# Optimization experiments

Measured on AMD Instinct MI355X. Metric: run time of the kernel, lower is better.

Reference implementation:

```python
import jax, jax.numpy as jnp
import numpy as np

R = 5.0      # cutoff radius (init arg)
N = 4096     # total atoms
B = 8        # number of periodic systems in the batch


def setup_inputs() -> dict:
    key = jax.random.key(0)
    k1, k2, k3 = jax.random.split(key, 3)
    # positions in a ~20 Angstrom box (matches cell scale)
    pos = jax.random.uniform(k1, (N, 3), dtype=jnp.float32) * 20.0
    # sorted per-atom graph ids, as produced by a batched molecular loader
    batch = jnp.sort(jax.random.randint(k2, (N,), 0, B))
    # near-cubic 20A cells with small triclinic perturbation (well-conditioned)
    cell = jnp.eye(3, dtype=jnp.float32) * 20.0 + 0.5 * jax.random.normal(k3, (B, 3, 3), dtype=jnp.float32)
    return {"pos": pos, "cell": cell, "batch": batch}


def reference(pos, cell, batch):
    # Dense, fixed-shape equivalent of RadiusGraph.forward with PBC cell wrap.
    # Original returns dynamically filtered (edge_index, disp); here we return
    # the full [N,N,3] displacement grid (masked to 0 off-graph) plus the
    # boolean edge mask -- same math, jit-compatible static shapes.
    n = pos.shape[0]
    disp = pos[:, None, :] - pos[None, :, :]            # [N,N,3], row i minus col j
    # PBC minimum-image wrap: per edge, cell is taken from the ROW node's graph
    cell_n = cell[batch]                                # [N,3,3]
    inv_cellT = jnp.linalg.inv(jnp.swapaxes(cell_n, 1, 2))   # [N,3,3] = (cell^T)^{-1}
    # scaled = solve(cell^T, disp) vectorized over all pairs
    scaled = jnp.einsum('iab,ijb->ija', inv_cellT, disp)     # [N,N,3]
    disp = disp - jnp.einsum('iab,ijb->ija', cell_n, jnp.round(scaled))
    # edge validity: same graph, no self-loop, within cutoff (after wrap)
    same_graph = batch[:, None] == batch[None, :]
    not_self = ~jnp.eye(n, dtype=bool)
    mask = same_graph & not_self & (jnp.linalg.norm(disp, axis=-1) < R)
    disp = jnp.where(mask[..., None], disp, jnp.zeros((), disp.dtype))
    return disp, mask
```

## Files before the change

kernel.cpp:

```cpp
#include <hip/hip_runtime.h>
#include <math.h>

#define NATOMS 4096
#define R_CUT 5.0f
#define BLOCK 256
#define GRID 2048
#define TPR (NATOMS / BLOCK)
#define NTILE (NATOMS * TPR)

typedef float f3 __attribute__((ext_vector_type(3), aligned(4)));

__global__ __launch_bounds__(BLOCK) void radius_graph_kernel(
    const float* __restrict__ pos,
    const float* __restrict__ cell,
    const int*   __restrict__ batch,
    float* __restrict__ disp_out,
    float* __restrict__ mask_out)
{
    const int tid = (int)threadIdx.x;

    for (int T = (int)blockIdx.x; T < NTILE; T += GRID) {
        const int i  = T >> 4;
        const int jb = T & (TPR - 1);
        const int j  = jb * BLOCK + tid;

        const int bi = batch[i];
        const float pix = pos[i * 3 + 0];
        const float piy = pos[i * 3 + 1];
        const float piz = pos[i * 3 + 2];

        const float* C = cell + (size_t)bi * 9;
        const float C00 = C[0], C01 = C[1], C02 = C[2];
        const float C10 = C[3], C11 = C[4], C12 = C[5];
        const float C20 = C[6], C21 = C[7], C22 = C[8];
        const float cof00 =  (C11 * C22 - C12 * C21);
        const float cof01 = -(C10 * C22 - C12 * C20);
        const float cof02 =  (C10 * C21 - C11 * C20);
        const float cof10 = -(C01 * C22 - C02 * C21);
        const float cof11 =  (C00 * C22 - C02 * C20);
        const float cof12 = -(C00 * C21 - C01 * C20);
        const float cof20 =  (C01 * C12 - C02 * C11);
        const float cof21 = -(C00 * C12 - C02 * C10);
        const float cof22 =  (C00 * C11 - C01 * C10);
        const float det = C00 * cof00 + C01 * cof01 + C02 * cof02;
        const float id  = 1.0f / det;
        const float A00 = cof00 * id, A01 = cof01 * id, A02 = cof02 * id;
        const float A10 = cof10 * id, A11 = cof11 * id, A12 = cof12 * id;
        const float A20 = cof20 * id, A21 = cof21 * id, A22 = cof22 * id;

        const float pjx = pos[j * 3 + 0];
        const float pjy = pos[j * 3 + 1];
        const float pjz = pos[j * 3 + 2];
        const int   bjv = batch[j];

        const float d0 = __fsub_rn(pix, pjx);
        const float d1 = __fsub_rn(piy, pjy);
        const float d2 = __fsub_rn(piz, pjz);

        const float s0 = __fadd_rn(__fadd_rn(__fmul_rn(A00, d0), __fmul_rn(A01, d1)), __fmul_rn(A02, d2));
        const float s1 = __fadd_rn(__fadd_rn(__fmul_rn(A10, d0), __fmul_rn(A11, d1)), __fmul_rn(A12, d2));
        const float s2 = __fadd_rn(__fadd_rn(__fmul_rn(A20, d0), __fmul_rn(A21, d1)), __fmul_rn(A22, d2));

        const float r0 = rintf(s0);
        const float r1 = rintf(s1);
        const float r2 = rintf(s2);

        const float w0 = __fsub_rn(d0, __fadd_rn(__fadd_rn(__fmul_rn(C00, r0), __fmul_rn(C01, r1)), __fmul_rn(C02, r2)));
        const float w1 = __fsub_rn(d1, __fadd_rn(__fadd_rn(__fmul_rn(C10, r0), __fmul_rn(C11, r1)), __fmul_rn(C12, r2)));
        const float w2 = __fsub_rn(d2, __fadd_rn(__fadd_rn(__fmul_rn(C20, r0), __fmul_rn(C21, r1)), __fmul_rn(C22, r2)));

        const float n2 = __fadd_rn(__fadd_rn(__fmul_rn(w0, w0), __fmul_rn(w1, w1)), __fmul_rn(w2, w2));
        const bool m = (bi == bjv) && (i != j) && (sqrtf(n2) < R_CUT);

        f3 v;
        v.x = m ? w0 : 0.0f;
        v.y = m ? w1 : 0.0f;
        v.z = m ? w2 : 0.0f;
        *(f3*)(disp_out + (size_t)T * (BLOCK * 3) + (size_t)tid * 3) = v;
        mask_out[(size_t)T * BLOCK + tid] = m ? 1.0f : 0.0f;
    }
}

extern "C" void kernel_launch(void* const* d_in, const int* in_sizes, int n_in,
                              void* d_out, int out_size, void* d_ws, size_t ws_size,
                              hipStream_t stream) {
    const float* pos   = (const float*)d_in[0];
    const float* cell  = (const float*)d_in[1];
    const int*   batch = (const int*)d_in[2];

    float* disp_out = (float*)d_out;
    float* mask_out = (float*)d_out + (size_t)NATOMS * NATOMS * 3;

    radius_graph_kernel<<<GRID, BLOCK, 0, stream>>>(pos, cell, batch, disp_out, mask_out);
}
```

Baseline: 262.7 us.

## Zero output with vectorized memset kernel, then scatter only valid edges

Splits the work into two kernels. The first bulk-zeroes the whole output with 16-byte stores. The second computes each row, skips pairs from different graphs, and writes displacement and mask only for edges within the cutoff. This replaces the dense 3-float unaligned stores with wide zero stores plus sparse scattered writes. The cost is an extra kernel launch and uncoalesced scattered stores.

```diff
diff --git a/kernel.cpp b/kernel.cpp
--- a/kernel.cpp
+++ b/kernel.cpp
@@ -4,54 +4,66 @@
 #define NATOMS 4096
 #define R_CUT 5.0f
 #define BLOCK 256
-#define GRID 2048
-#define TPR (NATOMS / BLOCK)
-#define NTILE (NATOMS * TPR)
 
+typedef float f4 __attribute__((ext_vector_type(4)));
 typedef float f3 __attribute__((ext_vector_type(3), aligned(4)));
 
-__global__ __launch_bounds__(BLOCK) void radius_graph_kernel(
+__global__ __launch_bounds__(BLOCK) void zero_kernel(f4* __restrict__ out, int n16)
+{
+    const int stride = (int)gridDim.x * BLOCK;
+    int idx = (int)blockIdx.x * BLOCK + (int)threadIdx.x;
+    const f4 z = {0.0f, 0.0f, 0.0f, 0.0f};
+    for (; idx < n16; idx += stride)
+        out[idx] = z;
+}
+
+__global__ __launch_bounds__(BLOCK) void sparse_kernel(
     const float* __restrict__ pos,
     const float* __restrict__ cell,
     const int*   __restrict__ batch,
     float* __restrict__ disp_out,
     float* __restrict__ mask_out)
 {
+    const int i   = (int)blockIdx.x;
     const int tid = (int)threadIdx.x;
 
-    for (int T = (int)blockIdx.x; T < NTILE; T += GRID) {
-        const int i  = T >> 4;
-        const int jb = T & (TPR - 1);
-        const int j  = jb * BLOCK + tid;
+    const int bi = batch[i];
+    const float pix = pos[i * 3 + 0];
+    const float piy = pos[i * 3 + 1];
+    const float piz = pos[i * 3 + 2];
 
-        const int bi = batch[i];
-        const float pix = pos[i * 3 + 0];
-        const float piy = pos[i * 3 + 1];
-        const float piz = pos[i * 3 + 2];
+    const float* C = cell + (size_t)bi * 9;
+    const float C00 = C[0], C01 = C[1], C02 = C[2];
+    const float C10 = C[3], C11 = C[4], C12 = C[5];
+    const float C20 = C[6], C21 = C[7], C22 = C[8];
+    const float cof00 =  (C11 * C22 - C12 * C21);
+    const float cof01 = -(C10 * C22 - C12 * C20);
+    const float cof02 =  (C10 * C21 - C11 * C20);
+    const float cof10 = -(C01 * C22 - C02 * C21);
+    const float cof11 =  (C00 * C22 - C02 * C20);
+    const float cof12 = -(C00 * C21 - C01 * C20);
+    const float cof20 =  (C01 * C12 - C02 * C11);
+    const float cof21 = -(C00 * C12 - C02 * C10);
+    const float cof22 =  (C00 * C11 - C01 * C10);
+    const float det = C00 * cof00 + C01 * cof01 + C02 * cof02;
+    const float id  = 1.0f / det;
+    const float A00 = cof00 * id, A01 = cof01 * id, A02 = cof02 * id;
+    const float A10 = cof10 * id, A11 = cof11 * id, A12 = cof12 * id;
+    const float A20 = cof20 * id, A21 = cof21 * id, A22 = cof22 * id;
 
-        const float* C = cell + (size_t)bi * 9;
-        const float C00 = C[0], C01 = C[1], C02 = C[2];
-        const float C10 = C[3], C11 = C[4], C12 = C[5];
-        const float C20 = C[6], C21 = C[7], C22 = C[8];
-        const float cof00 =  (C11 * C22 - C12 * C21);
-        const float cof01 = -(C10 * C22 - C12 * C20);
-        const float cof02 =  (C10 * C21 - C11 * C20);
-        const float cof10 = -(C01 * C22 - C02 * C21);
-        const float cof11 =  (C00 * C22 - C02 * C20);
-        const float cof12 = -(C00 * C21 - C01 * C20);
-        const float cof20 =  (C01 * C12 - C02 * C11);
-        const float cof21 = -(C00 * C12 - C02 * C10);
-        const float cof22 =  (C00 * C11 - C01 * C10);
-        const float det = C00 * cof00 + C01 * cof01 + C02 * cof02;
-        const float id  = 1.0f / det;
-        const float A00 = cof00 * id, A01 = cof01 * id, A02 = cof02 * id;
-        const float A10 = cof10 * id, A11 = cof11 * id, A12 = cof12 * id;
-        const float A20 = cof20 * id, A21 = cof21 * id, A22 = cof22 * id;
+    const size_t rowm = (size_t)i * NATOMS;
+    const size_t rowd = rowm * 3;
+
+    #pragma unroll 4
+    for (int k = 0; k < NATOMS / BLOCK; ++k) {
+        const int j = k * BLOCK + tid;
+
+        const int bjv = batch[j];
+        if (bjv != bi) continue;
 
         const float pjx = pos[j * 3 + 0];
         const float pjy = pos[j * 3 + 1];
         const float pjz = pos[j * 3 + 2];
-        const int   bjv = batch[j];
 
         const float d0 = __fsub_rn(pix, pjx);
         const float d1 = __fsub_rn(piy, pjy);
@@ -70,14 +82,13 @@
         const float w2 = __fsub_rn(d2, __fadd_rn(__fadd_rn(__fmul_rn(C20, r0), __fmul_rn(C21, r1)), __fmul_rn(C22, r2)));
 
         const float n2 = __fadd_rn(__fadd_rn(__fmul_rn(w0, w0), __fmul_rn(w1, w1)), __fmul_rn(w2, w2));
-        const bool m = (bi == bjv) && (i != j) && (sqrtf(n2) < R_CUT);
+        const bool m = (i != j) && (sqrtf(n2) < R_CUT);
 
-        f3 v;
-        v.x = m ? w0 : 0.0f;
-        v.y = m ? w1 : 0.0f;
-        v.z = m ? w2 : 0.0f;
-        *(f3*)(disp_out + (size_t)T * (BLOCK * 3) + (size_t)tid * 3) = v;
-        mask_out[(size_t)T * BLOCK + tid] = m ? 1.0f : 0.0f;
+        if (m) {
+            f3 v; v.x = w0; v.y = w1; v.z = w2;
+            *(f3*)(disp_out + rowd + (size_t)j * 3) = v;
+            mask_out[rowm + (size_t)j] = 1.0f;
+        }
     }
 }
 
@@ -91,5 +102,8 @@
     float* disp_out = (float*)d_out;
     float* mask_out = (float*)d_out + (size_t)NATOMS * NATOMS * 3;
 
-    radius_graph_kernel<<<GRID, BLOCK, 0, stream>>>(pos, cell, batch, disp_out, mask_out);
+    const int n16 = (NATOMS / 4) * NATOMS * 4;
+    zero_kernel<<<2048, BLOCK, 0, stream>>>((f4*)d_out, n16);
+
+    sparse_kernel<<<NATOMS, BLOCK, 0, stream>>>(pos, cell, batch, disp_out, mask_out);
 }
```

Result: slower. 277.4 us (+5.6%).
